# Kernel optimization log

Hardware: AMD Instinct MI355X
Metric: run time of the kernel (lower is better)

## Reference

```python
import jax, jax.numpy as jnp
import numpy as np


def _orthogonal_matrix(vectors):
    # Q = I @ H1 @ H2 @ ... ; each H = I - 2 v v^T applied as a rank-1 update:
    # Q @ H = Q - 2 (Q v) v^T  (same math as explicit matmul, O(d^2) per reflection)
    dim = vectors.shape[1]
    eye = jnp.eye(dim, dtype=vectors.dtype)

    def step(Q, v):
        vn = v / (jnp.linalg.norm(v) + 1e-8)
        Q = Q - 2.0 * jnp.outer(Q @ vn, vn)
        return Q, None

    Q, _ = jax.lax.scan(step, eye, vectors)
    return Q


def setup_inputs() -> dict:
    key = jax.random.key(0)
    k1, k2 = jax.random.split(key)
    dim, n_reflections, batch = 2048, 30, 16384
    x = jax.random.normal(k1, (batch, dim), dtype=jnp.float32)
    vectors = jax.random.normal(k2, (n_reflections, dim), dtype=jnp.float32)
    bias = jnp.zeros((dim,), dtype=jnp.float32)
    return {"x": x, "vectors": vectors, "bias": bias}


def reference(x, vectors, bias):
    Q = _orthogonal_matrix(vectors)      # [dim, dim]
    return x @ Q + bias                  # [batch, dim]
```

## Files before the change

### kernel.cpp

```cpp
#include <hip/hip_runtime.h>
#include <math.h>

#define DIM   2048
#define NREF  30
#define KPAD  32
#define BATCH 16384

typedef __attribute__((ext_vector_type(8))) short short8;
typedef __attribute__((ext_vector_type(4))) float f32x4;

#define WS_VN   0
#define WS_G    61440
#define WS_T    62464
#define WS_FP1  63488
#define WS_FP2  96256

__device__ __forceinline__ unsigned short f2bf(float f) {
    unsigned u = __float_as_uint(f);
    u += 0x7FFF + ((u >> 16) & 1);
    return (unsigned short)(u >> 16);
}

__global__ void k_prep(const float* __restrict__ vec, float* __restrict__ vn,
                       float* __restrict__ G) {
    int b = blockIdx.x, t = threadIdx.x;
    __shared__ float wsum[3][4];
    if (b < NREF) {
        const float* v = vec + b * DIM;
        float s = 0.f;
        for (int d = t; d < DIM; d += 256) { float xv = v[d]; s += xv * xv; }
        #pragma unroll
        for (int off = 32; off > 0; off >>= 1) s += __shfl_down(s, off);
        if ((t & 63) == 0) wsum[0][t >> 6] = s;
        __syncthreads();
        float tot = wsum[0][0] + wsum[0][1] + wsum[0][2] + wsum[0][3];
        float scale = 1.f / (sqrtf(tot) + 1e-8f);
        float* o = vn + b * DIM;
        for (int d = t; d < DIM; d += 256) o[d] = v[d] * scale;
    } else {
        int idx = b - NREF;
        int i = idx / NREF, j = idx % NREF;
        const float* a = vec + i * DIM;
        const float* c = vec + j * DIM;
        float sab = 0.f, saa = 0.f, sbb = 0.f;
        for (int d = t; d < DIM; d += 256) {
            float av = a[d], cv = c[d];
            sab += av * cv; saa += av * av; sbb += cv * cv;
        }
        #pragma unroll
        for (int off = 32; off > 0; off >>= 1) {
            sab += __shfl_down(sab, off);
            saa += __shfl_down(saa, off);
            sbb += __shfl_down(sbb, off);
        }
        if ((t & 63) == 0) { wsum[0][t >> 6] = sab; wsum[1][t >> 6] = saa; wsum[2][t >> 6] = sbb; }
        __syncthreads();
        if (t == 0) {
            float tab = wsum[0][0] + wsum[0][1] + wsum[0][2] + wsum[0][3];
            float taa = wsum[1][0] + wsum[1][1] + wsum[1][2] + wsum[1][3];
            float tbb = wsum[2][0] + wsum[2][1] + wsum[2][2] + wsum[2][3];
            G[i * NREF + j] = tab / ((sqrtf(taa) + 1e-8f) * (sqrtf(tbb) + 1e-8f));
        }
    }
}

__global__ void k_T2(const float* __restrict__ G, float* __restrict__ T) {
    int t = threadIdx.x;
    __shared__ float Gs[NREF * NREF];
    __shared__ float Ts[NREF][NREF];
    for (int idx = t; idx < NREF * NREF; idx += 64) {
        Gs[idx] = G[idx];
        Ts[idx / NREF][idx % NREF] = 0.f;
    }
    __syncthreads();
    if (t < NREF) {
        Ts[t][t] = 2.f;
        for (int j = t + 1; j < NREF; j++) {
            float val = 0.f;
            for (int mm = t; mm < j; mm++) val += Ts[t][mm] * Gs[mm * NREF + j];
            Ts[t][j] = -2.f * val;
        }
    }
    __syncthreads();
    for (int idx = t; idx < NREF * NREF; idx += 64) T[idx] = Ts[idx / NREF][idx % NREF];
}

__global__ void k_mid(const float* __restrict__ vn, const float* __restrict__ T,
                      unsigned short* __restrict__ fp1, unsigned short* __restrict__ fp2) {
    int b = blockIdx.x, t = threadIdx.x;
    if (b < 8) {
        __shared__ float W2s[256][33];
        int d = b * 256 + t;
        float vr[NREF];
        #pragma unroll
        for (int j = 0; j < NREF; j++) vr[j] = vn[j * DIM + d];
        #pragma unroll
        for (int k = 0; k < KPAD; k++) {
            float acc = 0.f;
            if (k < NREF)
                for (int j = 0; j <= k; j++) acc += vr[j] * T[j * NREF + k];
            W2s[t][k] = acc;
        }
        __syncthreads();
        short8* out = (short8*)fp1;
        #pragma unroll
        for (int u = 0; u < 4; u++) {
            int lf = t * 4 + u;
            int ks_l = lf >> 7, nt = (lf >> 6) & 1, lane = lf & 63;
            int q = lane >> 4, n = lane & 15;
            short8 v;
            #pragma unroll
            for (int j = 0; j < 8; j++)
                v[j] = (short)f2bf(W2s[ks_l * 32 + q * 8 + j][nt * 16 + n]);
            out[((b * 8 + ks_l) * 2 + nt) * 64 + lane] = v;
        }
    } else {
        int g = (b - 8) * 256 + t;
        int ct = g >> 6, lane = g & 63;
        int q = lane >> 4, n = lane & 15;
        short8 v;
        #pragma unroll
        for (int j = 0; j < 8; j++) {
            int k = q * 8 + j;
            float f = (k < NREF) ? vn[(size_t)k * DIM + ct * 16 + n] : 0.f;
            v[j] = (short)f2bf(f);
        }
        ((short8*)fp2)[ct * 64 + lane] = v;
    }
}

__global__ __launch_bounds__(256, 4) void k_fused(const float* __restrict__ x,
                                                  const short8* __restrict__ fp1,
                                                  const short8* __restrict__ fp2,
                                                  const float* __restrict__ bias,
                                                  float* __restrict__ y) {
    int tid = threadIdx.x;
    int wave = tid >> 6, lane = tid & 63;
    int m = lane & 15, q = lane >> 4;
    int r0 = blockIdx.x * 16;
    int kb = wave * 512;

    const float* xp = x + (size_t)(r0 + m) * DIM + kb + q * 8;

    f32x4 acc0 = {0.f, 0.f, 0.f, 0.f};
    f32x4 acc1 = {0.f, 0.f, 0.f, 0.f};
    #pragma unroll 4
    for (int ks = 0; ks < 16; ks++) {
        f32x4 xa = *(const f32x4*)(xp + ks * 32);
        f32x4 xb = *(const f32x4*)(xp + ks * 32 + 4);
        short8 a;
        a[0] = (short)f2bf(xa[0]); a[1] = (short)f2bf(xa[1]);
        a[2] = (short)f2bf(xa[2]); a[3] = (short)f2bf(xa[3]);
        a[4] = (short)f2bf(xb[0]); a[5] = (short)f2bf(xb[1]);
        a[6] = (short)f2bf(xb[2]); a[7] = (short)f2bf(xb[3]);
        int ksg = wave * 16 + ks;
        short8 b0 = fp1[(ksg * 2 + 0) * 64 + lane];
        short8 b1 = fp1[(ksg * 2 + 1) * 64 + lane];
        acc0 = __builtin_amdgcn_mfma_f32_16x16x32_bf16(a, b0, acc0, 0, 0, 0);
        acc1 = __builtin_amdgcn_mfma_f32_16x16x32_bf16(a, b1, acc1, 0, 0, 0);
    }

    __shared__ f32x4 red[4][64][2];
    __shared__ unsigned short Slds[16][32];
    red[wave][lane][0] = acc0;
    red[wave][lane][1] = acc1;
    __syncthreads();
    if (tid < 64) {
        f32x4 s0 = red[0][tid][0], s1 = red[0][tid][1];
        #pragma unroll
        for (int w = 1; w < 4; w++) { s0 += red[w][tid][0]; s1 += red[w][tid][1]; }
        int mq = tid & 15, qq = tid >> 4;
        #pragma unroll
        for (int reg = 0; reg < 4; reg++) {
            Slds[qq * 4 + reg][mq]      = f2bf(s0[reg]);
            Slds[qq * 4 + reg][16 + mq] = f2bf(s1[reg]);
        }
    }
    __syncthreads();

    short8 aS = *(const short8*)&Slds[m][q * 8];
    f32x4 zero = {0.f, 0.f, 0.f, 0.f};
    int c0 = wave * 512;
    int rbase = r0 + q * 4;

    #pragma unroll 4
    for (int t = 0; t < 32; t += 2) {
        short8 b0 = fp2[(wave * 32 + t) * 64 + lane];
        short8 b1 = fp2[(wave * 32 + t + 1) * 64 + lane];
        f32x4 p0 = __builtin_amdgcn_mfma_f32_16x16x32_bf16(aS, b0, zero, 0, 0, 0);
        f32x4 p1 = __builtin_amdgcn_mfma_f32_16x16x32_bf16(aS, b1, zero, 0, 0, 0);
        int cc0 = c0 + t * 16 + m;
        int cc1 = cc0 + 16;
        float bi0 = bias[cc0];
        float bi1 = bias[cc1];
        const float* xc0 = x + (size_t)rbase * DIM + cc0;
        const float* xc1 = x + (size_t)rbase * DIM + cc1;
        float* yc0 = y + (size_t)rbase * DIM + cc0;
        float* yc1 = y + (size_t)rbase * DIM + cc1;
        #pragma unroll
        for (int reg = 0; reg < 4; reg++) {
            yc0[(size_t)reg * DIM] = xc0[(size_t)reg * DIM] + bi0 - p0[reg];
            yc1[(size_t)reg * DIM] = xc1[(size_t)reg * DIM] + bi1 - p1[reg];
        }
    }
}

extern "C" void kernel_launch(void* const* d_in, const int* in_sizes, int n_in,
                              void* d_out, int out_size, void* d_ws, size_t ws_size,
                              hipStream_t stream) {
    const float* x    = (const float*)d_in[0];
    const float* vec  = (const float*)d_in[1];
    const float* bias = (const float*)d_in[2];
    float* out = (float*)d_out;
    float* ws  = (float*)d_ws;

    float* vn = ws + WS_VN;
    float* G  = ws + WS_G;
    float* T  = ws + WS_T;
    unsigned short* fp1 = (unsigned short*)(ws + WS_FP1);
    unsigned short* fp2 = (unsigned short*)(ws + WS_FP2);

    k_prep<<<NREF + NREF * NREF, 256, 0, stream>>>(vec, vn, G);
    k_T2<<<1, 64, 0, stream>>>(G, T);
    k_mid<<<40, 256, 0, stream>>>(vn, T, fp1, fp2);
    k_fused<<<BATCH / 16, 256, 0, stream>>>(x, (const short8*)fp1, (const short8*)fp2, bias, out);
}
```

Before: 277.9 us.

## Stage x rows in LDS via direct global-to-LDS loads and reuse for epilogue

The fused kernel now copies a block of 8 rows of x into shared memory using global_load_lds with an XOR swizzle, then reads x from LDS both for the projection MFMA and for the residual epilogue. Before, x was read from global memory twice. Rows per block drop from 16 to 8, so half of the MFMA rows are wasted padding, and 64KB of LDS per block lowers the occupancy hint to 2. The goal is to remove the second global read of x in exchange for lower occupancy and idle MFMA lanes.

```diff
diff --git a/kernel.cpp b/kernel.cpp
--- a/kernel.cpp
+++ b/kernel.cpp
@@ -5,9 +5,13 @@
 #define NREF  30
 #define KPAD  32
 #define BATCH 16384
+#define ROWS  8
 
 typedef __attribute__((ext_vector_type(8))) short short8;
 typedef __attribute__((ext_vector_type(4))) float f32x4;
+
+typedef const __attribute__((address_space(1))) void* gas1_t;
+typedef __attribute__((address_space(3))) void* las3_t;
 
 #define WS_VN   0
 #define WS_G    61440
@@ -129,25 +133,47 @@
     }
 }
 
-__global__ __launch_bounds__(256, 4) void k_fused(const float* __restrict__ x,
+__global__ __launch_bounds__(256, 2) void k_fused(const float* __restrict__ x,
                                                   const short8* __restrict__ fp1,
                                                   const short8* __restrict__ fp2,
                                                   const float* __restrict__ bias,
                                                   float* __restrict__ y) {
+    __shared__ float xs[ROWS * DIM];
+    __shared__ f32x4 red[4][32][2];
+    __shared__ unsigned short Slds[ROWS][KPAD];
+
     int tid = threadIdx.x;
     int wave = tid >> 6, lane = tid & 63;
     int m = lane & 15, q = lane >> 4;
-    int r0 = blockIdx.x * 16;
+    int r0 = blockIdx.x * ROWS;
+    char* lbase = (char*)xs;
+
+    {
+        const char* xbase = (const char*)(x + (size_t)r0 * DIM);
+        #pragma unroll
+        for (int i = 0; i < 16; i++) {
+            int s = wave * 16 + i;
+            int r = s >> 3, j = s & 7;
+            unsigned gin = ((unsigned)(j * 1024 + lane * 16)) ^ ((unsigned)(r << 4));
+            const char* g = xbase + (size_t)r * (DIM * 4) + gin;
+            __builtin_amdgcn_global_load_lds((gas1_t)g, (las3_t)(lbase + s * 1024),
+                                             16, 0, 0);
+        }
+    }
+    asm volatile("s_waitcnt vmcnt(0)" ::: "memory");
+    __syncthreads();
+
     int kb = wave * 512;
-
-    const float* xp = x + (size_t)(r0 + m) * DIM + kb + q * 8;
-
+    int lr = m & 7;
+    unsigned rowbase = (unsigned)lr * (DIM * 4);
+    unsigned sw = (unsigned)(lr << 4);
     f32x4 acc0 = {0.f, 0.f, 0.f, 0.f};
     f32x4 acc1 = {0.f, 0.f, 0.f, 0.f};
     #pragma unroll 4
     for (int ks = 0; ks < 16; ks++) {
-        f32x4 xa = *(const f32x4*)(xp + ks * 32);
-        f32x4 xb = *(const f32x4*)(xp + ks * 32 + 4);
+        unsigned o = (unsigned)((kb + ks * 32 + q * 8) * 4);
+        f32x4 xa = *(const f32x4*)(lbase + rowbase + (o ^ sw));
+        f32x4 xb = *(const f32x4*)(lbase + rowbase + ((o + 16) ^ sw));
         short8 a;
         a[0] = (short)f2bf(xa[0]); a[1] = (short)f2bf(xa[1]);
         a[2] = (short)f2bf(xa[2]); a[3] = (short)f2bf(xa[3]);
@@ -160,12 +186,9 @@
         acc1 = __builtin_amdgcn_mfma_f32_16x16x32_bf16(a, b1, acc1, 0, 0, 0);
     }
 
-    __shared__ f32x4 red[4][64][2];
-    __shared__ unsigned short Slds[16][32];
-    red[wave][lane][0] = acc0;
-    red[wave][lane][1] = acc1;
-    __syncthreads();
-    if (tid < 64) {
+    if (lane < 32) { red[wave][lane][0] = acc0; red[wave][lane][1] = acc1; }
+    __syncthreads();
+    if (tid < 32) {
         f32x4 s0 = red[0][tid][0], s1 = red[0][tid][1];
         #pragma unroll
         for (int w = 1; w < 4; w++) { s0 += red[w][tid][0]; s1 += red[w][tid][1]; }
@@ -178,10 +201,9 @@
     }
     __syncthreads();
 
-    short8 aS = *(const short8*)&Slds[m][q * 8];
+    short8 aS = *(const short8*)&Slds[m & 7][q * 8];
     f32x4 zero = {0.f, 0.f, 0.f, 0.f};
     int c0 = wave * 512;
-    int rbase = r0 + q * 4;
 
     #pragma unroll 4
     for (int t = 0; t < 32; t += 2) {
@@ -193,14 +215,17 @@
         int cc1 = cc0 + 16;
         float bi0 = bias[cc0];
         float bi1 = bias[cc1];
-        const float* xc0 = x + (size_t)rbase * DIM + cc0;
-        const float* xc1 = x + (size_t)rbase * DIM + cc1;
-        float* yc0 = y + (size_t)rbase * DIM + cc0;
-        float* yc1 = y + (size_t)rbase * DIM + cc1;
-        #pragma unroll
-        for (int reg = 0; reg < 4; reg++) {
-            yc0[(size_t)reg * DIM] = xc0[(size_t)reg * DIM] + bi0 - p0[reg];
-            yc1[(size_t)reg * DIM] = xc1[(size_t)reg * DIM] + bi1 - p1[reg];
+        if (q < 2) {
+            #pragma unroll
+            for (int reg = 0; reg < 4; reg++) {
+                int lrr = q * 4 + reg;
+                unsigned rb = (unsigned)lrr * (DIM * 4);
+                unsigned swr = (unsigned)(lrr << 4);
+                float xv0 = *(const float*)(lbase + rb + (((unsigned)(cc0 * 4)) ^ swr));
+                float xv1 = *(const float*)(lbase + rb + (((unsigned)(cc1 * 4)) ^ swr));
+                y[(size_t)(r0 + lrr) * DIM + cc0] = xv0 + bi0 - p0[reg];
+                y[(size_t)(r0 + lrr) * DIM + cc1] = xv1 + bi1 - p1[reg];
+            }
         }
     }
 }
@@ -223,5 +248,5 @@
     k_prep<<<NREF + NREF * NREF, 256, 0, stream>>>(vec, vn, G);
     k_T2<<<1, 64, 0, stream>>>(G, T);
     k_mid<<<40, 256, 0, stream>>>(vn, T, fp1, fp2);
-    k_fused<<<BATCH / 16, 256, 0, stream>>>(x, (const short8*)fp1, (const short8*)fp2, bias, out);
-}
+    k_fused<<<BATCH / ROWS, 256, 0, stream>>>(x, (const short8*)fp1, (const short8*)fp2, bias, out);
+}
```

Result: slower. 290.4 us (+4.5%).

## Split fused kernel into projection and fp32 VALU rank-30 update passes

Applied to the files above, without the earlier changes.

The single fused kernel is split in two. The first pass computes the 32-wide projection S = x·W via MFMA and writes it in fp32 to the workspace. A second kernel reloads x and applies y = x + bias - S·Vn using fp32 VALU FMAs, with per-thread register-cached vn columns and an LDS tile of S. This removes the bf16 MFMA second stage and improves store coalescing, at the cost of reading x a second time and one more kernel launch.

```diff
diff --git a/kernel.cpp b/kernel.cpp
--- a/kernel.cpp
+++ b/kernel.cpp
@@ -8,12 +8,13 @@
 
 typedef __attribute__((ext_vector_type(8))) short short8;
 typedef __attribute__((ext_vector_type(4))) float f32x4;
+typedef __attribute__((ext_vector_type(2))) float f32x2;
 
 #define WS_VN   0
 #define WS_G    61440
 #define WS_T    62464
 #define WS_FP1  63488
-#define WS_FP2  96256
+#define WS_S    96256
 
 __device__ __forceinline__ unsigned short f2bf(float f) {
     unsigned u = __float_as_uint(f);
@@ -86,54 +87,38 @@
 }
 
 __global__ void k_mid(const float* __restrict__ vn, const float* __restrict__ T,
-                      unsigned short* __restrict__ fp1, unsigned short* __restrict__ fp2) {
+                      unsigned short* __restrict__ fp1) {
     int b = blockIdx.x, t = threadIdx.x;
-    if (b < 8) {
-        __shared__ float W2s[256][33];
-        int d = b * 256 + t;
-        float vr[NREF];
-        #pragma unroll
-        for (int j = 0; j < NREF; j++) vr[j] = vn[j * DIM + d];
-        #pragma unroll
-        for (int k = 0; k < KPAD; k++) {
-            float acc = 0.f;
-            if (k < NREF)
-                for (int j = 0; j <= k; j++) acc += vr[j] * T[j * NREF + k];
-            W2s[t][k] = acc;
-        }
-        __syncthreads();
-        short8* out = (short8*)fp1;
-        #pragma unroll
-        for (int u = 0; u < 4; u++) {
-            int lf = t * 4 + u;
-            int ks_l = lf >> 7, nt = (lf >> 6) & 1, lane = lf & 63;
-            int q = lane >> 4, n = lane & 15;
-            short8 v;
-            #pragma unroll
-            for (int j = 0; j < 8; j++)
-                v[j] = (short)f2bf(W2s[ks_l * 32 + q * 8 + j][nt * 16 + n]);
-            out[((b * 8 + ks_l) * 2 + nt) * 64 + lane] = v;
-        }
-    } else {
-        int g = (b - 8) * 256 + t;
-        int ct = g >> 6, lane = g & 63;
+    __shared__ float W2s[256][33];
+    int d = b * 256 + t;
+    float vr[NREF];
+    #pragma unroll
+    for (int j = 0; j < NREF; j++) vr[j] = vn[j * DIM + d];
+    #pragma unroll
+    for (int k = 0; k < KPAD; k++) {
+        float acc = 0.f;
+        if (k < NREF)
+            for (int j = 0; j <= k; j++) acc += vr[j] * T[j * NREF + k];
+        W2s[t][k] = acc;
+    }
+    __syncthreads();
+    short8* out = (short8*)fp1;
+    #pragma unroll
+    for (int u = 0; u < 4; u++) {
+        int lf = t * 4 + u;
+        int ks_l = lf >> 7, nt = (lf >> 6) & 1, lane = lf & 63;
         int q = lane >> 4, n = lane & 15;
         short8 v;
         #pragma unroll
-        for (int j = 0; j < 8; j++) {
-            int k = q * 8 + j;
-            float f = (k < NREF) ? vn[(size_t)k * DIM + ct * 16 + n] : 0.f;
-            v[j] = (short)f2bf(f);
-        }
-        ((short8*)fp2)[ct * 64 + lane] = v;
-    }
-}
-
-__global__ __launch_bounds__(256, 4) void k_fused(const float* __restrict__ x,
-                                                  const short8* __restrict__ fp1,
-                                                  const short8* __restrict__ fp2,
-                                                  const float* __restrict__ bias,
-                                                  float* __restrict__ y) {
+        for (int j = 0; j < 8; j++)
+            v[j] = (short)f2bf(W2s[ks_l * 32 + q * 8 + j][nt * 16 + n]);
+        out[((b * 8 + ks_l) * 2 + nt) * 64 + lane] = v;
+    }
+}
+
+__global__ __launch_bounds__(256) void k_p1(const float* __restrict__ x,
+                                            const short8* __restrict__ fp1,
+                                            float* __restrict__ S) {
     int tid = threadIdx.x;
     int wave = tid >> 6, lane = tid & 63;
     int m = lane & 15, q = lane >> 4;
@@ -161,7 +146,6 @@
     }
 
     __shared__ f32x4 red[4][64][2];
-    __shared__ unsigned short Slds[16][32];
     red[wave][lane][0] = acc0;
     red[wave][lane][1] = acc1;
     __syncthreads();
@@ -172,36 +156,48 @@
         int mq = tid & 15, qq = tid >> 4;
         #pragma unroll
         for (int reg = 0; reg < 4; reg++) {
-            Slds[qq * 4 + reg][mq]      = f2bf(s0[reg]);
-            Slds[qq * 4 + reg][16 + mq] = f2bf(s1[reg]);
-        }
-    }
-    __syncthreads();
-
-    short8 aS = *(const short8*)&Slds[m][q * 8];
-    f32x4 zero = {0.f, 0.f, 0.f, 0.f};
-    int c0 = wave * 512;
-    int rbase = r0 + q * 4;
-
+            size_t row = r0 + qq * 4 + reg;
+            S[row * KPAD + mq]      = s0[reg];
+            S[row * KPAD + 16 + mq] = s1[reg];
+        }
+    }
+}
+
+__global__ __launch_bounds__(256) void k_p2(const float* __restrict__ x,
+                                            const float* __restrict__ S,
+                                            const float* __restrict__ vn,
+                                            const float* __restrict__ bias,
+                                            float* __restrict__ y) {
+    __shared__ float Stile[32 * KPAD];
+    int tid = threadIdx.x;
+    int wave = tid >> 6, lane = tid & 63;
+    int rc = blockIdx.x >> 2;
+    int cg = blockIdx.x & 3;
+    int r0 = rc * 32;
+    int cl = cg * 512 + wave * 128 + lane * 2;
+
+    ((f32x4*)Stile)[tid] = ((const f32x4*)(S + (size_t)r0 * KPAD))[tid];
+
+    f32x2 vt[NREF];
+    #pragma unroll
+    for (int n = 0; n < NREF; n++)
+        vt[n] = *(const f32x2*)(vn + n * DIM + cl);
+    f32x2 bi = *(const f32x2*)(bias + cl);
+    __syncthreads();
+
+    const float* xp = x + (size_t)r0 * DIM + cl;
+    float* yp = y + (size_t)r0 * DIM + cl;
     #pragma unroll 4
-    for (int t = 0; t < 32; t += 2) {
-        short8 b0 = fp2[(wave * 32 + t) * 64 + lane];
-        short8 b1 = fp2[(wave * 32 + t + 1) * 64 + lane];
-        f32x4 p0 = __builtin_amdgcn_mfma_f32_16x16x32_bf16(aS, b0, zero, 0, 0, 0);
-        f32x4 p1 = __builtin_amdgcn_mfma_f32_16x16x32_bf16(aS, b1, zero, 0, 0, 0);
-        int cc0 = c0 + t * 16 + m;
-        int cc1 = cc0 + 16;
-        float bi0 = bias[cc0];
-        float bi1 = bias[cc1];
-        const float* xc0 = x + (size_t)rbase * DIM + cc0;
-        const float* xc1 = x + (size_t)rbase * DIM + cc1;
-        float* yc0 = y + (size_t)rbase * DIM + cc0;
-        float* yc1 = y + (size_t)rbase * DIM + cc1;
-        #pragma unroll
-        for (int reg = 0; reg < 4; reg++) {
-            yc0[(size_t)reg * DIM] = xc0[(size_t)reg * DIM] + bi0 - p0[reg];
-            yc1[(size_t)reg * DIM] = xc1[(size_t)reg * DIM] + bi1 - p1[reg];
-        }
+    for (int r = 0; r < 32; r++) {
+        f32x2 xv = *(const f32x2*)(xp + (size_t)r * DIM);
+        f32x2 acc = xv + bi;
+        const float* Sr = &Stile[r * KPAD];
+        #pragma unroll
+        for (int n = 0; n < NREF; n++) {
+            float sn = Sr[n];
+            acc -= sn * vt[n];
+        }
+        *(f32x2*)(yp + (size_t)r * DIM) = acc;
     }
 }
 
@@ -218,10 +214,11 @@
     float* G  = ws + WS_G;
     float* T  = ws + WS_T;
     unsigned short* fp1 = (unsigned short*)(ws + WS_FP1);
-    unsigned short* fp2 = (unsigned short*)(ws + WS_FP2);
+    float* S = ws + WS_S;
 
     k_prep<<<NREF + NREF * NREF, 256, 0, stream>>>(vec, vn, G);
     k_T2<<<1, 64, 0, stream>>>(G, T);
-    k_mid<<<40, 256, 0, stream>>>(vn, T, fp1, fp2);
-    k_fused<<<BATCH / 16, 256, 0, stream>>>(x, (const short8*)fp1, (const short8*)fp2, bias, out);
-}
+    k_mid<<<8, 256, 0, stream>>>(vn, T, fp1);
+    k_p1<<<BATCH / 16, 256, 0, stream>>>(x, (const short8*)fp1, S);
+    k_p2<<<2048, 256, 0, stream>>>(x, S, vn, bias, out);
+}
```

New measurement: 290.8 us. +4.6%, slower.
